# Performance work log

Hardware: AMD Instinct MI355X
Metric: run time of the kernel (lower is better)

## Reference

```python
import jax, jax.numpy as jnp
import numpy as np

EMBED_DIM = 1024
NUM_HEADS = 16
HEAD_DIM = EMBED_DIM // NUM_HEADS  # 64
B, NQ, NK = 4, 1024, 2048


def setup_inputs() -> dict:
    key = jax.random.key(0)
    ks = jax.random.split(key, 13)
    s = 1.0 / np.sqrt(EMBED_DIM)
    inp = {
        "query": jax.random.normal(ks[0], (B, NQ, EMBED_DIM), jnp.float32),
        "key": jax.random.normal(ks[1], (B, NK, EMBED_DIM), jnp.float32),
        "value": jax.random.normal(ks[2], (B, NK, EMBED_DIM), jnp.float32),
        # positive multiplicity weights per key element
        "key_multiplicities": jax.random.uniform(ks[3], (B, NK), jnp.float32, 0.1, 4.0),
        "wq_w": jax.random.normal(ks[4], (EMBED_DIM, EMBED_DIM), jnp.float32) * s,
        "wq_b": jnp.zeros((EMBED_DIM,), jnp.float32),
        "wk_w": jax.random.normal(ks[5], (EMBED_DIM, EMBED_DIM), jnp.float32) * s,
        "wk_b": jnp.zeros((EMBED_DIM,), jnp.float32),
        "wv_w": jax.random.normal(ks[6], (EMBED_DIM, EMBED_DIM), jnp.float32) * s,
        "wv_b": jnp.zeros((EMBED_DIM,), jnp.float32),
        "wo_w": jax.random.normal(ks[7], (EMBED_DIM, EMBED_DIM), jnp.float32) * s,
        "wo_b": jnp.zeros((EMBED_DIM,), jnp.float32),
    }
    return inp


def _split_heads(x, b, n):
    # (b, n, h*d) -> (b, h, n, d)
    return x.reshape(b, n, NUM_HEADS, HEAD_DIM).transpose(0, 2, 1, 3)


def reference(query, key, value, key_multiplicities,
              wq_w, wq_b, wk_w, wk_b, wv_w, wv_b, wo_w, wo_b):
    b, n_q, _ = query.shape
    _, n_k, _ = key.shape
    q = _split_heads(query @ wq_w.T + wq_b, b, n_q)   # (b, h, n_q, d)
    k = _split_heads(key @ wk_w.T + wk_b, b, n_k)     # (b, h, n_k, d)
    v = _split_heads(value @ wv_w.T + wv_b, b, n_k)   # (b, h, n_k, d)
    scale = 1.0 / jnp.sqrt(jnp.asarray(HEAD_DIM, q.dtype))
    scores = jnp.einsum("bhqd,bhkd->bhqk", q, k) * scale
    # multiplicities weight each key: softmax_i(m_i * exp(s_i)) == softmax(s_i + log m_i)
    logits = scores + jnp.log(key_multiplicities)[:, None, None, :]
    attn = jax.nn.softmax(logits, axis=-1)            # (b, h, n_q, n_k)
    out = jnp.einsum("bhqk,bhkd->bhqd", attn, v)
    out = out.transpose(0, 2, 1, 3).reshape(b, n_q, NUM_HEADS * HEAD_DIM)
    return out @ wo_w.T + wo_b
```

## Files before the change

### kernel.cpp

```cpp
#include <hip/hip_runtime.h>
#include <hip/hip_bf16.h>
#include <stdint.h>
#include <stddef.h>

typedef __attribute__((ext_vector_type(8))) short bf16x8;
typedef __attribute__((ext_vector_type(4))) short short4v;
typedef __attribute__((ext_vector_type(4))) float f32x4;
typedef __attribute__((ext_vector_type(2))) uint32_t u32x2;
typedef __attribute__((ext_vector_type(4))) uint32_t u32x4;

#define MFMA16(a, b, c) __builtin_amdgcn_mfma_f32_16x16x32_bf16((a), (b), (c), 0, 0, 0)

__device__ __forceinline__ short f2bf(float f) {
    uint32_t u = __builtin_bit_cast(uint32_t, f);
    u = (u + 0x7FFFu + ((u >> 16) & 1u)) >> 16;
    return (short)(uint16_t)u;
}

__device__ __forceinline__ uint32_t pkbf(float a, float b) {
#if __has_builtin(__builtin_amdgcn_cvt_pk_bf16_f32)
    auto r = __builtin_amdgcn_cvt_pk_bf16_f32(a, b);
    return __builtin_bit_cast(uint32_t, r);
#else
    return (uint32_t)(uint16_t)f2bf(a) | ((uint32_t)(uint16_t)f2bf(b) << 16);
#endif
}

__device__ __forceinline__ float fexp2(float x) {
#if __has_builtin(__builtin_amdgcn_exp2f)
    return __builtin_amdgcn_exp2f(x);
#else
    return exp2f(x);
#endif
}

__device__ __forceinline__ void gload16(const short* g, short* l) {
    __builtin_amdgcn_global_load_lds(
        (const __attribute__((address_space(1))) unsigned int*)g,
        (__attribute__((address_space(3))) unsigned int*)l, 16, 0, 0);
}

__global__ __launch_bounds__(256) void prep_kernel(
        const float* __restrict__ w0, const float* __restrict__ w1,
        const float* __restrict__ w2, const float* __restrict__ w3,
        const float* __restrict__ q, const float* __restrict__ k,
        const float* __restrict__ v, const float* __restrict__ m,
        short* __restrict__ wb, short* __restrict__ Qa,
        short* __restrict__ Ka, short* __restrict__ Va,
        float* __restrict__ lm) {
    const int bid = blockIdx.x;
    if (bid >= 12288) {
        const int i = ((bid - 12288) * 256 + threadIdx.x) * 8;
        f32x4 a = *(const f32x4*)(m + i);
        f32x4 b = *(const f32x4*)(m + i + 4);
        f32x4 oa, ob;
        #pragma unroll
        for (int j = 0; j < 4; ++j) { oa[j] = __log2f(a[j]); ob[j] = __log2f(b[j]); }
        *(f32x4*)(lm + i) = oa;
        *(f32x4*)(lm + i + 4) = ob;
        return;
    }
    const float* src;
    short* dst;
    int local;
    if (bid < 2048) {
        const int z = bid >> 9;
        local = bid & 511;
        src = (z == 0) ? w0 : (z == 1) ? w1 : (z == 2) ? w2 : w3;
        dst = wb + (size_t)z * 1048576;
    } else if (bid < 4096) { src = q; dst = Qa; local = bid - 2048; }
    else if (bid < 8192)   { src = k; dst = Ka; local = bid - 4096; }
    else                   { src = v; dst = Va; local = bid - 8192; }
    const size_t i = ((size_t)local * 256 + threadIdx.x) * 8;
    f32x4 a = *(const f32x4*)(src + i);
    f32x4 b = *(const f32x4*)(src + i + 4);
    u32x4 o = { pkbf(a[0], a[1]), pkbf(a[2], a[3]), pkbf(b[0], b[1]), pkbf(b[2], b[3]) };
    *(u32x4*)(dst + i) = o;
}

__global__ __launch_bounds__(256) void proj_kernel(
        const short* __restrict__ Qa, const short* __restrict__ Ka,
        const short* __restrict__ Va, const short* __restrict__ wb,
        const float* __restrict__ wq_b, const float* __restrict__ wk_b,
        const float* __restrict__ wv_b, short* __restrict__ Qp,
        short* __restrict__ Kp, short* __restrict__ Vt, const int ybase) {
    __shared__ short As[4][128 * 32];
    __shared__ short Bs[4][128 * 32];

    const int cpx = gridDim.x >> 3;
    const int l = (blockIdx.x & 7) * cpx + (blockIdx.x >> 3);
    const int y = (l >> 3) + ybase;
    const int tn = (l & 7) * 128;

    const short* A; const short* W; const float* bias; int mode, tm;
    if (y < 32)      { A = Qa; W = wb;           bias = wq_b; mode = 0; tm = y * 128; }
    else if (y < 96) { A = Ka; W = wb + 1048576; bias = wk_b; mode = 1; tm = (y - 32) * 128; }
    else             { A = Va; W = wb + 2097152; bias = wv_b; mode = 2; tm = (y - 96) * 128; }

    const int t = threadIdx.x, lane = t & 63, w = t >> 6;
    const int wr = w >> 1, wc = w & 1;
    const int qd = lane >> 4, c = lane & 15;

    f32x4 acc[4][4];
    #pragma unroll
    for (int i = 0; i < 4; ++i)
        #pragma unroll
        for (int j = 0; j < 4; ++j) acc[i][j] = (f32x4){0.f, 0.f, 0.f, 0.f};

    const int r0 = w * 16 + (lane >> 2);
    const int qc = (lane & 3) ^ ((lane >> 3) & 3);
    const short* ga0 = A + (size_t)(tm + r0) * 1024 + qc * 8;
    const short* ga1 = ga0 + 64 * 1024;
    const short* gb0 = W + (size_t)(tn + r0) * 1024 + qc * 8;
    const short* gb1 = gb0 + 64 * 1024;
    const int lofs = w * 512;
    const int swz = (qd ^ ((c >> 1) & 3)) * 8;

    for (int k0 = 0; k0 < 1024; k0 += 128) {
        __syncthreads();
        #pragma unroll
        for (int kh = 0; kh < 4; ++kh) {
            gload16(ga0 + k0 + kh * 32, &As[kh][lofs]);
            gload16(ga1 + k0 + kh * 32, &As[kh][lofs + 2048]);
            gload16(gb0 + k0 + kh * 32, &Bs[kh][lofs]);
            gload16(gb1 + k0 + kh * 32, &Bs[kh][lofs + 2048]);
        }
        __syncthreads();
        #pragma unroll
        for (int kh = 0; kh < 4; ++kh) {
            bf16x8 af[4], bfr[4];
            #pragma unroll
            for (int rt = 0; rt < 4; ++rt)
                af[rt] = *(const bf16x8*)&As[kh][(wr * 64 + rt * 16 + c) * 32 + swz];
            #pragma unroll
            for (int ct = 0; ct < 4; ++ct)
                bfr[ct] = *(const bf16x8*)&Bs[kh][(wc * 64 + ct * 16 + c) * 32 + swz];
            #pragma unroll
            for (int rt = 0; rt < 4; ++rt)
                #pragma unroll
                for (int ct = 0; ct < 4; ++ct)
                    acc[rt][ct] = MFMA16(af[rt], bfr[ct], acc[rt][ct]);
        }
    }

    float bv[4];
    #pragma unroll
    for (int ct = 0; ct < 4; ++ct) bv[ct] = bias[tn + wc * 64 + ct * 16 + c];

    if (mode == 2) {
        #pragma unroll
        for (int rt = 0; rt < 4; ++rt)
            #pragma unroll
            for (int ct = 0; ct < 4; ++ct) {
                const int cg = tn + wc * 64 + ct * 16 + c;
                const int h = cg >> 6, d = cg & 63;
                const int rg0 = tm + wr * 64 + rt * 16 + qd * 4;
                const int bb = rg0 >> 11, n = rg0 & 2047;
                u32x2 pk = { pkbf(acc[rt][ct][0] + bv[ct], acc[rt][ct][1] + bv[ct]),
                             pkbf(acc[rt][ct][2] + bv[ct], acc[rt][ct][3] + bv[ct]) };
                *(u32x2*)&Vt[((((size_t)(bb * 16 + h)) * 64 + d) << 11) + n] = pk;
            }
    } else {
        short* out = (mode == 0) ? Qp : Kp;
        const int nshift = (mode == 0) ? 10 : 11;
        const int mask = (1 << nshift) - 1;
        #pragma unroll
        for (int rt = 0; rt < 4; ++rt)
            #pragma unroll
            for (int ct = 0; ct < 4; ++ct) {
                const int cg = tn + wc * 64 + ct * 16 + c;
                const int h = cg >> 6, d = cg & 63;
                #pragma unroll
                for (int r = 0; r < 4; ++r) {
                    const int rg = tm + wr * 64 + rt * 16 + qd * 4 + r;
                    const int bb = rg >> nshift, n = rg & mask;
                    out[((((size_t)(bb * 16 + h)) << nshift) + n) * 64 + d] =
                        f2bf(acc[rt][ct][r] + bv[ct]);
                }
            }
    }
}

__global__ __launch_bounds__(256, 4) void gemm_o_kernel(
        const short* __restrict__ Ob, const short* __restrict__ W,
        const float* __restrict__ bias, float* __restrict__ out) {
    __shared__ short As[4][128 * 32];
    __shared__ short Bs[4][64 * 32];

    const int cpx = gridDim.x >> 3;
    const int l = (blockIdx.x & 7) * cpx + (blockIdx.x >> 3);
    const int tm = (l >> 4) * 128, tn = (l & 15) * 64;

    const int t = threadIdx.x, lane = t & 63, w = t >> 6;
    const int wr = w >> 1, wc = w & 1;
    const int qd = lane >> 4, c = lane & 15;

    f32x4 acc[4][2];
    #pragma unroll
    for (int i = 0; i < 4; ++i)
        #pragma unroll
        for (int j = 0; j < 2; ++j) acc[i][j] = (f32x4){0.f, 0.f, 0.f, 0.f};

    const int r0 = w * 16 + (lane >> 2);
    const int qc = (lane & 3) ^ ((lane >> 3) & 3);
    const short* ga0 = Ob + (size_t)(tm + r0) * 1024 + qc * 8;
    const short* ga1 = ga0 + 64 * 1024;
    const short* gb0 = W + (size_t)(tn + r0) * 1024 + qc * 8;
    const int lofs = w * 512;
    const int swz = (qd ^ ((c >> 1) & 3)) * 8;

    for (int k0 = 0; k0 < 1024; k0 += 128) {
        __syncthreads();
        #pragma unroll
        for (int kh = 0; kh < 4; ++kh) {
            gload16(ga0 + k0 + kh * 32, &As[kh][lofs]);
            gload16(ga1 + k0 + kh * 32, &As[kh][lofs + 2048]);
            gload16(gb0 + k0 + kh * 32, &Bs[kh][lofs]);
        }
        __syncthreads();
        #pragma unroll
        for (int kh = 0; kh < 4; ++kh) {
            bf16x8 af[4], bfr[2];
            #pragma unroll
            for (int rt = 0; rt < 4; ++rt)
                af[rt] = *(const bf16x8*)&As[kh][(wr * 64 + rt * 16 + c) * 32 + swz];
            #pragma unroll
            for (int ct = 0; ct < 2; ++ct)
                bfr[ct] = *(const bf16x8*)&Bs[kh][(wc * 32 + ct * 16 + c) * 32 + swz];
            #pragma unroll
            for (int rt = 0; rt < 4; ++rt)
                #pragma unroll
                for (int ct = 0; ct < 2; ++ct)
                    acc[rt][ct] = MFMA16(af[rt], bfr[ct], acc[rt][ct]);
        }
    }

    float bv[2];
    #pragma unroll
    for (int ct = 0; ct < 2; ++ct) bv[ct] = bias[tn + wc * 32 + ct * 16 + c];

    #pragma unroll
    for (int rt = 0; rt < 4; ++rt)
        #pragma unroll
        for (int ct = 0; ct < 2; ++ct) {
            const int cg = tn + wc * 32 + ct * 16 + c;
            #pragma unroll
            for (int r = 0; r < 4; ++r) {
                const int rg = tm + wr * 64 + rt * 16 + qd * 4 + r;
                out[(size_t)rg * 1024 + cg] = acc[rt][ct][r] + bv[ct];
            }
        }
}

__global__ __launch_bounds__(256, 2) void attn_kernel(
        const short* __restrict__ Qp, const short* __restrict__ Kp,
        const short* __restrict__ Vt, const float* __restrict__ logm,
        short* __restrict__ Ob) {
    __shared__ short Ps[128 * 128];
    __shared__ short Vs[64 * 128];
    __shared__ float Lm[128];
    short* Ks = Ps;

    const int bid = blockIdx.x;
    const int xcd = bid & 7, ii = bid >> 3;
    const int qt = ii >> 3, bh = xcd + ((ii & 7) << 3);
    const int b = bh >> 4;
    const int t = threadIdx.x, lane = t & 63, w = t >> 6;
    const int qd = lane >> 4, c = lane & 15;
    const int cl = c & 7;
    const float SC = 0.18033688011112042f;

    bf16x8 qf[2][2];
    #pragma unroll
    for (int ct = 0; ct < 2; ++ct)
        #pragma unroll
        for (int kd = 0; kd < 2; ++kd)
            qf[ct][kd] = *(const bf16x8*)(Qp +
                ((size_t)bh * 1024 + qt * 128 + w * 32 + ct * 16 + c) * 64 + kd * 32 + qd * 8);

    bf16x8 onesf;
    {
        const short ov = (c == 0) ? (short)0x3F80 : (short)0;
        #pragma unroll
        for (int j = 0; j < 8; ++j) onesf[j] = ov;
    }

    f32x4 oacc[2][5];
    #pragma unroll
    for (int i = 0; i < 2; ++i)
        #pragma unroll
        for (int j = 0; j < 5; ++j) oacc[i][j] = (f32x4){0.f, 0.f, 0.f, 0.f};

    const short* kgp[4];
    short* klp[4];
    const short* vgp[4];
    short* vlp[4];
    {
        const int krow = lane >> 3;
        const int kchk = (lane & 7) ^ krow;
        const int vrow = lane >> 4;
        #pragma unroll
        for (int i = 0; i < 4; ++i) {
            const int rk = w * 32 + i * 8 + krow;
            kgp[i] = Kp + ((size_t)bh * 2048 + rk) * 64 + kchk * 8;
            klp[i] = &Ks[(w * 4 + i) * 512];
            const int rv = w * 16 + i * 4 + vrow;
            const int vchk = (lane & 15) ^ (rv & 7);
            vgp[i] = Vt + ((size_t)bh * 64 + rv) * 2048 + vchk * 8;
            vlp[i] = &Vs[(w * 4 + i) * 512];
        }
    }

    for (int kt = 0; kt < 16; ++kt) {
        #pragma unroll
        for (int i = 0; i < 4; ++i) {
            gload16(kgp[i] + (size_t)kt * 8192, klp[i]);
            gload16(vgp[i] + kt * 128, vlp[i]);
        }
        if (t < 128) Lm[t] = logm[b * 2048 + kt * 128 + t];
        __syncthreads();

        f32x4 s[8][2];
        #pragma unroll
        for (int rt = 0; rt < 8; ++rt) {
            bf16x8 a0 = *(const bf16x8*)&Ks[(rt * 16 + c) * 64 + (qd ^ cl) * 8];
            bf16x8 a1 = *(const bf16x8*)&Ks[(rt * 16 + c) * 64 + ((4 | qd) ^ cl) * 8];
            #pragma unroll
            for (int ct = 0; ct < 2; ++ct) {
                f32x4 z = (f32x4){0.f, 0.f, 0.f, 0.f};
                s[rt][ct] = MFMA16(a1, qf[ct][1], MFMA16(a0, qf[ct][0], z));
            }
        }
        __syncthreads();

        #pragma unroll
        for (int rt = 0; rt < 8; ++rt) {
            f32x4 lv = *(const f32x4*)&Lm[rt * 16 + qd * 4];
            #pragma unroll
            for (int ct = 0; ct < 2; ++ct) {
                float p0 = fexp2(__builtin_fmaf(s[rt][ct][0], SC, lv[0]));
                float p1 = fexp2(__builtin_fmaf(s[rt][ct][1], SC, lv[1]));
                float p2 = fexp2(__builtin_fmaf(s[rt][ct][2], SC, lv[2]));
                float p3 = fexp2(__builtin_fmaf(s[rt][ct][3], SC, lv[3]));
                u32x2 pk = { pkbf(p0, p1), pkbf(p2, p3) };
                const int prow = w * 32 + ct * 16 + c;
                const int pch = (2 * rt + (qd >> 1)) ^ cl;
                *(u32x2*)&Ps[prow * 128 + pch * 8 + (qd & 1) * 4] = pk;
            }
        }

        #pragma unroll
        for (int kk = 0; kk < 4; ++kk) {
            const int lch = ((kk * 4 + qd) ^ cl) * 8;
            bf16x8 pf[2], vf[4];
            #pragma unroll
            for (int rtq = 0; rtq < 2; ++rtq)
                pf[rtq] = *(const bf16x8*)&Ps[(w * 32 + rtq * 16 + c) * 128 + lch];
            #pragma unroll
            for (int ct = 0; ct < 4; ++ct)
                vf[ct] = *(const bf16x8*)&Vs[(ct * 16 + c) * 128 + lch];
            #pragma unroll
            for (int rtq = 0; rtq < 2; ++rtq) {
                #pragma unroll
                for (int ct = 0; ct < 4; ++ct)
                    oacc[rtq][ct] = MFMA16(pf[rtq], vf[ct], oacc[rtq][ct]);
                oacc[rtq][4] = MFMA16(pf[rtq], onesf, oacc[rtq][4]);
            }
        }
        __syncthreads();
    }

    const int h = bh & 15;
    float inv[2][4];
    #pragma unroll
    for (int rtq = 0; rtq < 2; ++rtq)
        #pragma unroll
        for (int r = 0; r < 4; ++r)
            inv[rtq][r] = 1.f / __shfl(oacc[rtq][4][r], qd * 16);
    #pragma unroll
    for (int rtq = 0; rtq < 2; ++rtq)
        #pragma unroll
        for (int ct = 0; ct < 4; ++ct)
            #pragma unroll
            for (int r = 0; r < 4; ++r) {
                const int qg = qt * 128 + w * 32 + rtq * 16 + qd * 4 + r;
                const int e = h * 64 + ct * 16 + c;
                Ob[((size_t)(b * 1024 + qg)) * 1024 + e] = f2bf(oacc[rtq][ct][r] * inv[rtq][r]);
            }
}

extern "C" void kernel_launch(void* const* d_in, const int* in_sizes, int n_in,
                              void* d_out, int out_size, void* d_ws, size_t ws_size,
                              hipStream_t stream) {
    (void)in_sizes; (void)n_in; (void)out_size;
    const float* query = (const float*)d_in[0];
    const float* key   = (const float*)d_in[1];
    const float* value = (const float*)d_in[2];
    const float* mult  = (const float*)d_in[3];
    const float* wq_w  = (const float*)d_in[4];
    const float* wq_b  = (const float*)d_in[5];
    const float* wk_w  = (const float*)d_in[6];
    const float* wk_b  = (const float*)d_in[7];
    const float* wv_w  = (const float*)d_in[8];
    const float* wv_b  = (const float*)d_in[9];
    const float* wo_w  = (const float*)d_in[10];
    const float* wo_b  = (const float*)d_in[11];
    float* out = (float*)d_out;

    char* ws = (char*)d_ws;
    const size_t MB = 1024 * 1024;
    const bool merged = ws_size >= 89 * MB;

    short* wb = (short*)(ws + 0 * MB);
    short* Qa = (short*)(ws + 8 * MB);
    short* Ka = (short*)(ws + 16 * MB);
    short* Va = (short*)(ws + 32 * MB);
    short* Qp = (short*)(ws + 48 * MB);
    short* Kp = (short*)(ws + 56 * MB);
    short *Vt, *Ob; float* lm;
    if (merged) {
        Vt = (short*)(ws + 72 * MB);
        Ob = (short*)(ws + 8 * MB);
        lm = (float*)(ws + 88 * MB);
    } else {
        Vt = (short*)(ws + 8 * MB);
        Ob = (short*)(ws + 32 * MB);
        lm = (float*)(ws + 72 * MB);
    }

    prep_kernel<<<dim3(12292), 256, 0, stream>>>(
        wq_w, wk_w, wv_w, wo_w, query, key, value, mult, wb, Qa, Ka, Va, lm);
    if (merged) {
        proj_kernel<<<dim3(1280), 256, 0, stream>>>(
            Qa, Ka, Va, wb, wq_b, wk_b, wv_b, Qp, Kp, Vt, 0);
    } else {
        proj_kernel<<<dim3(768), 256, 0, stream>>>(
            Qa, Ka, Va, wb, wq_b, wk_b, wv_b, Qp, Kp, Vt, 0);
        proj_kernel<<<dim3(512), 256, 0, stream>>>(
            Qa, Ka, Va, wb, wq_b, wk_b, wv_b, Qp, Kp, Vt, 96);
    }
    attn_kernel<<<dim3(512), 256, 0, stream>>>(Qp, Kp, Vt, lm, Ob);
    gemm_o_kernel<<<dim3(512), 256, 0, stream>>>(Ob, wb + 3145728, wo_b, out);
}
```

Baseline: 273.4 us.

## Double-buffer LDS tiles in projection and output GEMMs to overlap loads

Both GEMM kernels now split the K loop into 64-wide stages held in two LDS buffers. The next stage's global-to-LDS loads are issued before the current stage is computed, with explicit vmcnt waits and s_barrier calls in place of two __syncthreads per 128-wide step. The aim is to hide global memory latency behind MFMA work without growing LDS. In exchange there are twice as many loop iterations, and correctness depends on the hand-counted vmcnt values.

```diff
diff --git a/kernel.cpp b/kernel.cpp
--- a/kernel.cpp
+++ b/kernel.cpp
@@ -84,8 +84,8 @@
         const float* __restrict__ wq_b, const float* __restrict__ wk_b,
         const float* __restrict__ wv_b, short* __restrict__ Qp,
         short* __restrict__ Kp, short* __restrict__ Vt, const int ybase) {
-    __shared__ short As[4][128 * 32];
-    __shared__ short Bs[4][128 * 32];
+    __shared__ short As[2][2][4096];
+    __shared__ short Bs[2][2][4096];
 
     const int cpx = gridDim.x >> 3;
     const int l = (blockIdx.x & 7) * cpx + (blockIdx.x >> 3);
@@ -116,32 +116,45 @@
     const int lofs = w * 512;
     const int swz = (qd ^ ((c >> 1) & 3)) * 8;
 
-    for (int k0 = 0; k0 < 1024; k0 += 128) {
-        __syncthreads();
-        #pragma unroll
-        for (int kh = 0; kh < 4; ++kh) {
-            gload16(ga0 + k0 + kh * 32, &As[kh][lofs]);
-            gload16(ga1 + k0 + kh * 32, &As[kh][lofs + 2048]);
-            gload16(gb0 + k0 + kh * 32, &Bs[kh][lofs]);
-            gload16(gb1 + k0 + kh * 32, &Bs[kh][lofs + 2048]);
-        }
-        __syncthreads();
-        #pragma unroll
-        for (int kh = 0; kh < 4; ++kh) {
+    auto stage = [&](int buf, int k0) {
+        #pragma unroll
+        for (int kh = 0; kh < 2; ++kh) {
+            gload16(ga0 + k0 + kh * 32, &As[buf][kh][lofs]);
+            gload16(ga1 + k0 + kh * 32, &As[buf][kh][lofs + 2048]);
+            gload16(gb0 + k0 + kh * 32, &Bs[buf][kh][lofs]);
+            gload16(gb1 + k0 + kh * 32, &Bs[buf][kh][lofs + 2048]);
+        }
+    };
+    auto compute = [&](int buf) {
+        #pragma unroll
+        for (int kh = 0; kh < 2; ++kh) {
             bf16x8 af[4], bfr[4];
             #pragma unroll
             for (int rt = 0; rt < 4; ++rt)
-                af[rt] = *(const bf16x8*)&As[kh][(wr * 64 + rt * 16 + c) * 32 + swz];
+                af[rt] = *(const bf16x8*)&As[buf][kh][(wr * 64 + rt * 16 + c) * 32 + swz];
             #pragma unroll
             for (int ct = 0; ct < 4; ++ct)
-                bfr[ct] = *(const bf16x8*)&Bs[kh][(wc * 64 + ct * 16 + c) * 32 + swz];
+                bfr[ct] = *(const bf16x8*)&Bs[buf][kh][(wc * 64 + ct * 16 + c) * 32 + swz];
             #pragma unroll
             for (int rt = 0; rt < 4; ++rt)
                 #pragma unroll
                 for (int ct = 0; ct < 4; ++ct)
                     acc[rt][ct] = MFMA16(af[rt], bfr[ct], acc[rt][ct]);
         }
-    }
+    };
+
+    stage(0, 0);
+    #pragma unroll 1
+    for (int it = 0; it < 15; ++it) {
+        stage((it + 1) & 1, (it + 1) * 64);
+        asm volatile("s_waitcnt vmcnt(8)" ::: "memory");
+        __builtin_amdgcn_s_barrier();
+        compute(it & 1);
+        __builtin_amdgcn_s_barrier();
+    }
+    asm volatile("s_waitcnt vmcnt(0)" ::: "memory");
+    __builtin_amdgcn_s_barrier();
+    compute(1);
 
     float bv[4];
     #pragma unroll
@@ -184,8 +197,8 @@
 __global__ __launch_bounds__(256, 4) void gemm_o_kernel(
         const short* __restrict__ Ob, const short* __restrict__ W,
         const float* __restrict__ bias, float* __restrict__ out) {
-    __shared__ short As[4][128 * 32];
-    __shared__ short Bs[4][64 * 32];
+    __shared__ short As[2][2][4096];
+    __shared__ short Bs[2][2][2048];
 
     const int cpx = gridDim.x >> 3;
     const int l = (blockIdx.x & 7) * cpx + (blockIdx.x >> 3);
@@ -207,33 +220,48 @@
     const short* ga1 = ga0 + 64 * 1024;
     const short* gb0 = W + (size_t)(tn + r0) * 1024 + qc * 8;
     const int lofs = w * 512;
+    const int lofsb = (w & 3) * 512;
     const int swz = (qd ^ ((c >> 1) & 3)) * 8;
 
-    for (int k0 = 0; k0 < 1024; k0 += 128) {
-        __syncthreads();
-        #pragma unroll
-        for (int kh = 0; kh < 4; ++kh) {
-            gload16(ga0 + k0 + kh * 32, &As[kh][lofs]);
-            gload16(ga1 + k0 + kh * 32, &As[kh][lofs + 2048]);
-            gload16(gb0 + k0 + kh * 32, &Bs[kh][lofs]);
-        }
-        __syncthreads();
-        #pragma unroll
-        for (int kh = 0; kh < 4; ++kh) {
+    auto stage = [&](int buf, int k0) {
+        #pragma unroll
+        for (int kh = 0; kh < 2; ++kh) {
+            gload16(ga0 + k0 + kh * 32, &As[buf][kh][lofs]);
+            gload16(ga1 + k0 + kh * 32, &As[buf][kh][lofs + 2048]);
+            if (w < 4) gload16(gb0 + k0 + kh * 32, &Bs[buf][kh][lofsb]);
+        }
+    };
+    auto compute = [&](int buf) {
+        #pragma unroll
+        for (int kh = 0; kh < 2; ++kh) {
             bf16x8 af[4], bfr[2];
             #pragma unroll
             for (int rt = 0; rt < 4; ++rt)
-                af[rt] = *(const bf16x8*)&As[kh][(wr * 64 + rt * 16 + c) * 32 + swz];
+                af[rt] = *(const bf16x8*)&As[buf][kh][(wr * 64 + rt * 16 + c) * 32 + swz];
             #pragma unroll
             for (int ct = 0; ct < 2; ++ct)
-                bfr[ct] = *(const bf16x8*)&Bs[kh][(wc * 32 + ct * 16 + c) * 32 + swz];
+                bfr[ct] = *(const bf16x8*)&Bs[buf][kh][(wc * 32 + ct * 16 + c) * 32 + swz];
             #pragma unroll
             for (int rt = 0; rt < 4; ++rt)
                 #pragma unroll
                 for (int ct = 0; ct < 2; ++ct)
                     acc[rt][ct] = MFMA16(af[rt], bfr[ct], acc[rt][ct]);
         }
-    }
+    };
+
+    stage(0, 0);
+    #pragma unroll 1
+    for (int it = 0; it < 15; ++it) {
+        stage((it + 1) & 1, (it + 1) * 64);
+        if (w < 4) asm volatile("s_waitcnt vmcnt(6)" ::: "memory");
+        else       asm volatile("s_waitcnt vmcnt(4)" ::: "memory");
+        __builtin_amdgcn_s_barrier();
+        compute(it & 1);
+        __builtin_amdgcn_s_barrier();
+    }
+    asm volatile("s_waitcnt vmcnt(0)" ::: "memory");
+    __builtin_amdgcn_s_barrier();
+    compute(1);
 
     float bv[2];
     #pragma unroll
```

Measured after the change: 278.2 us. No clear change (+1.8%).

## Fuse fp32-to-bf16 activation conversion into the projection GEMM A-tile load

Applied to the files above, without the earlier changes.

The prep kernel no longer converts query/key/value to bf16 in a separate pass. The projection kernel now reads fp32 activations directly, converts them to bf16 in registers and writes them to LDS, while weights still go through global_load_lds. This removes a full write-and-reread of the bf16 activation copies and simplifies the workspace layout. The cost is that A-tile loads become synchronous register loads and the fp32 activations are reloaded by each of the 8 column tiles, so loads overlap less with compute.

```diff
diff --git a/kernel.cpp b/kernel.cpp
--- a/kernel.cpp
+++ b/kernel.cpp
@@ -43,14 +43,11 @@
 __global__ __launch_bounds__(256) void prep_kernel(
         const float* __restrict__ w0, const float* __restrict__ w1,
         const float* __restrict__ w2, const float* __restrict__ w3,
-        const float* __restrict__ q, const float* __restrict__ k,
-        const float* __restrict__ v, const float* __restrict__ m,
-        short* __restrict__ wb, short* __restrict__ Qa,
-        short* __restrict__ Ka, short* __restrict__ Va,
+        const float* __restrict__ m, short* __restrict__ wb,
         float* __restrict__ lm) {
     const int bid = blockIdx.x;
-    if (bid >= 12288) {
-        const int i = ((bid - 12288) * 256 + threadIdx.x) * 8;
+    if (bid >= 2048) {
+        const int i = ((bid - 2048) * 256 + threadIdx.x) * 8;
         f32x4 a = *(const f32x4*)(m + i);
         f32x4 b = *(const f32x4*)(m + i + 4);
         f32x4 oa, ob;
@@ -60,17 +57,10 @@
         *(f32x4*)(lm + i + 4) = ob;
         return;
     }
-    const float* src;
-    short* dst;
-    int local;
-    if (bid < 2048) {
-        const int z = bid >> 9;
-        local = bid & 511;
-        src = (z == 0) ? w0 : (z == 1) ? w1 : (z == 2) ? w2 : w3;
-        dst = wb + (size_t)z * 1048576;
-    } else if (bid < 4096) { src = q; dst = Qa; local = bid - 2048; }
-    else if (bid < 8192)   { src = k; dst = Ka; local = bid - 4096; }
-    else                   { src = v; dst = Va; local = bid - 8192; }
+    const int z = bid >> 9;
+    const int local = bid & 511;
+    const float* src = (z == 0) ? w0 : (z == 1) ? w1 : (z == 2) ? w2 : w3;
+    short* dst = wb + (size_t)z * 1048576;
     const size_t i = ((size_t)local * 256 + threadIdx.x) * 8;
     f32x4 a = *(const f32x4*)(src + i);
     f32x4 b = *(const f32x4*)(src + i + 4);
@@ -79,23 +69,23 @@
 }
 
 __global__ __launch_bounds__(256) void proj_kernel(
-        const short* __restrict__ Qa, const short* __restrict__ Ka,
-        const short* __restrict__ Va, const short* __restrict__ wb,
+        const float* __restrict__ Qf, const float* __restrict__ Kf,
+        const float* __restrict__ Vf, const short* __restrict__ wb,
         const float* __restrict__ wq_b, const float* __restrict__ wk_b,
         const float* __restrict__ wv_b, short* __restrict__ Qp,
-        short* __restrict__ Kp, short* __restrict__ Vt, const int ybase) {
-    __shared__ short As[4][128 * 32];
-    __shared__ short Bs[4][128 * 32];
+        short* __restrict__ Kp, short* __restrict__ Vt) {
+    __shared__ short As[4][4096];
+    __shared__ short Bs[4][4096];
 
     const int cpx = gridDim.x >> 3;
     const int l = (blockIdx.x & 7) * cpx + (blockIdx.x >> 3);
-    const int y = (l >> 3) + ybase;
+    const int y = l >> 3;
     const int tn = (l & 7) * 128;
 
-    const short* A; const short* W; const float* bias; int mode, tm;
-    if (y < 32)      { A = Qa; W = wb;           bias = wq_b; mode = 0; tm = y * 128; }
-    else if (y < 96) { A = Ka; W = wb + 1048576; bias = wk_b; mode = 1; tm = (y - 32) * 128; }
-    else             { A = Va; W = wb + 2097152; bias = wv_b; mode = 2; tm = (y - 96) * 128; }
+    const float* A; const short* W; const float* bias; int mode, tm;
+    if (y < 32)      { A = Qf; W = wb;           bias = wq_b; mode = 0; tm = y * 128; }
+    else if (y < 96) { A = Kf; W = wb + 1048576; bias = wk_b; mode = 1; tm = (y - 32) * 128; }
+    else             { A = Vf; W = wb + 2097152; bias = wv_b; mode = 2; tm = (y - 96) * 128; }
 
     const int t = threadIdx.x, lane = t & 63, w = t >> 6;
     const int wr = w >> 1, wc = w & 1;
@@ -109,8 +99,8 @@
 
     const int r0 = w * 16 + (lane >> 2);
     const int qc = (lane & 3) ^ ((lane >> 3) & 3);
-    const short* ga0 = A + (size_t)(tm + r0) * 1024 + qc * 8;
-    const short* ga1 = ga0 + 64 * 1024;
+    const float* gaf0 = A + (size_t)(tm + r0) * 1024 + qc * 8;
+    const float* gaf1 = gaf0 + 64 * 1024;
     const short* gb0 = W + (size_t)(tn + r0) * 1024 + qc * 8;
     const short* gb1 = gb0 + 64 * 1024;
     const int lofs = w * 512;
@@ -120,10 +110,21 @@
         __syncthreads();
         #pragma unroll
         for (int kh = 0; kh < 4; ++kh) {
-            gload16(ga0 + k0 + kh * 32, &As[kh][lofs]);
-            gload16(ga1 + k0 + kh * 32, &As[kh][lofs + 2048]);
             gload16(gb0 + k0 + kh * 32, &Bs[kh][lofs]);
             gload16(gb1 + k0 + kh * 32, &Bs[kh][lofs + 2048]);
+        }
+        #pragma unroll
+        for (int kh = 0; kh < 4; ++kh) {
+            f32x4 a0 = *(const f32x4*)(gaf0 + k0 + kh * 32);
+            f32x4 a1 = *(const f32x4*)(gaf0 + k0 + kh * 32 + 4);
+            f32x4 b0 = *(const f32x4*)(gaf1 + k0 + kh * 32);
+            f32x4 b1 = *(const f32x4*)(gaf1 + k0 + kh * 32 + 4);
+            u32x4 pa = { pkbf(a0[0], a0[1]), pkbf(a0[2], a0[3]),
+                         pkbf(a1[0], a1[1]), pkbf(a1[2], a1[3]) };
+            u32x4 pb = { pkbf(b0[0], b0[1]), pkbf(b0[2], b0[3]),
+                         pkbf(b1[0], b1[1]), pkbf(b1[2], b1[3]) };
+            *(u32x4*)&As[kh][lofs + lane * 8]        = pa;
+            *(u32x4*)&As[kh][lofs + 2048 + lane * 8] = pb;
         }
         __syncthreads();
         #pragma unroll
@@ -392,7 +393,7 @@
 extern "C" void kernel_launch(void* const* d_in, const int* in_sizes, int n_in,
                               void* d_out, int out_size, void* d_ws, size_t ws_size,
                               hipStream_t stream) {
-    (void)in_sizes; (void)n_in; (void)out_size;
+    (void)in_sizes; (void)n_in; (void)out_size; (void)ws_size;
     const float* query = (const float*)d_in[0];
     const float* key   = (const float*)d_in[1];
     const float* value = (const float*)d_in[2];
@@ -409,36 +410,17 @@
 
     char* ws = (char*)d_ws;
     const size_t MB = 1024 * 1024;
-    const bool merged = ws_size >= 89 * MB;
-
     short* wb = (short*)(ws + 0 * MB);
-    short* Qa = (short*)(ws + 8 * MB);
-    short* Ka = (short*)(ws + 16 * MB);
-    short* Va = (short*)(ws + 32 * MB);
-    short* Qp = (short*)(ws + 48 * MB);
-    short* Kp = (short*)(ws + 56 * MB);
-    short *Vt, *Ob; float* lm;
-    if (merged) {
-        Vt = (short*)(ws + 72 * MB);
-        Ob = (short*)(ws + 8 * MB);
-        lm = (float*)(ws + 88 * MB);
-    } else {
-        Vt = (short*)(ws + 8 * MB);
-        Ob = (short*)(ws + 32 * MB);
-        lm = (float*)(ws + 72 * MB);
-    }
-
-    prep_kernel<<<dim3(12292), 256, 0, stream>>>(
-        wq_w, wk_w, wv_w, wo_w, query, key, value, mult, wb, Qa, Ka, Va, lm);
-    if (merged) {
-        proj_kernel<<<dim3(1280), 256, 0, stream>>>(
-            Qa, Ka, Va, wb, wq_b, wk_b, wv_b, Qp, Kp, Vt, 0);
-    } else {
-        proj_kernel<<<dim3(768), 256, 0, stream>>>(
-            Qa, Ka, Va, wb, wq_b, wk_b, wv_b, Qp, Kp, Vt, 0);
-        proj_kernel<<<dim3(512), 256, 0, stream>>>(
-            Qa, Ka, Va, wb, wq_b, wk_b, wv_b, Qp, Kp, Vt, 96);
-    }
+    short* Qp = (short*)(ws + 8 * MB);
+    short* Kp = (short*)(ws + 16 * MB);
+    short* Vt = (short*)(ws + 32 * MB);
+    short* Ob = (short*)(ws + 48 * MB);
+    float* lm = (float*)(ws + 56 * MB);
+
+    prep_kernel<<<dim3(2052), 256, 0, stream>>>(
+        wq_w, wk_w, wv_w, wo_w, mult, wb, lm);
+    proj_kernel<<<dim3(1280), 256, 0, stream>>>(
+        query, key, value, wb, wq_b, wk_b, wv_b, Qp, Kp, Vt);
     attn_kernel<<<dim3(512), 256, 0, stream>>>(Qp, Kp, Vt, lm, Ob);
     gemm_o_kernel<<<dim3(512), 256, 0, stream>>>(Ob, wb + 3145728, wo_b, out);
 }
```

Result: slower. 293.4 us (+7.3%).
